# Performance work log

Hardware: AMD Instinct MI355X
Metric: run time of the kernel (lower is better)

The kernel has to match this reference:

```python
import jax, jax.numpy as jnp
import numpy as np

N_GRAPHS = 8
NODES_PER_G = 4096
N = N_GRAPHS * NODES_PER_G        # 32768 total nodes in the batched graph
E = N * 16                        # 524288 edges (avg degree 16)
F_IN = 128
HID = 64
FC_HID = 128
OUT = 2
SLOPE = 0.01                      # torch LeakyReLU default


def leaky_relu(x):
    return jnp.where(x >= 0, x, SLOPE * x)


def gcn_conv(x, W, b, src, dst, w, n_nodes):
    """PyG GCNConv with edge_weight: x' = D^-1/2 (A+I) D^-1/2 (x W) + b.
    Self-loops added with weight 1 (PyG default fill_value)."""
    xw = x @ W                                         # [N, out]
    deg = jax.ops.segment_sum(w, dst, num_segments=n_nodes) + 1.0  # +1 self-loop
    dinv = jnp.where(deg > 0, jax.lax.rsqrt(deg), 0.0)
    norm = dinv[src] * w * dinv[dst]                   # [E]
    agg = jax.ops.segment_sum(xw[src] * norm[:, None], dst, num_segments=n_nodes)
    agg = agg + xw * (dinv * dinv)[:, None]            # self-loop contribution
    return agg + b


def setup_inputs() -> dict:
    key = jax.random.key(0)
    ks = jax.random.split(key, 11)
    s = 0.05
    return {
        "x": jax.random.normal(ks[0], (N, F_IN), jnp.float32),
        "edge_index": jax.random.randint(ks[1], (2, E), 0, N, dtype=jnp.int32),
        "edge_attr": jax.random.uniform(ks[2], (E, 2), jnp.float32),
        "W1": jax.random.normal(ks[3], (F_IN, HID), jnp.float32) * s,
        "b1": jnp.zeros((HID,), jnp.float32),
        "W2": jax.random.normal(ks[4], (HID, 1), jnp.float32) * s,
        "b2": jnp.zeros((1,), jnp.float32),
        "fc1_W": jax.random.normal(ks[5], (NODES_PER_G, FC_HID), jnp.float32) * s,
        "fc1_b": jnp.zeros((FC_HID,), jnp.float32),
        "fc2_W": jax.random.normal(ks[6], (FC_HID, OUT), jnp.float32) * s,
        "fc2_b": jnp.zeros((OUT,), jnp.float32),
        "num_graphs": N_GRAPHS,
    }


def reference(x, edge_index, edge_attr, W1, b1, W2, b2, fc1_W, fc1_b, fc2_W, fc2_b, num_graphs):
    src, dst = edge_index[0], edge_index[1]
    w = edge_attr[:, 0]
    n = x.shape[0]
    h = leaky_relu(gcn_conv(x, W1, b1, src, dst, w, n))   # [N, 64]
    h = leaky_relu(gcn_conv(h, W2, b2, src, dst, w, n))   # [N, 1]
    out = h.reshape(num_graphs, -1)                       # [G, nodes_per_graph]
    out = leaky_relu(out @ fc1_W + fc1_b)                 # [G, 128]
    out = out @ fc2_W + fc2_b                             # [G, out_channels]
    return jax.nn.softmax(out, axis=1)
```

## Files before the change

kernel.cpp:

```cpp
#include <hip/hip_runtime.h>
#include <hip/hip_fp16.h>

#define F_IN 128
#define HID 64
#define FC_HID 128
#define NOUT 2
#define NGR 8
#define SLOPE 0.01f
#define SLOTS 64
#define NPB 256
#define NBUCK 256
#define DPB 128
#define SCAP 32
#define SEPT 8
#define ROWS_PB 16
#define XS_STR 132

__global__ __launch_bounds__(256) void fused_pg_kernel(const int* __restrict__ src,
                                                       const int* __restrict__ dst,
                                                       const float* __restrict__ edge_attr,
                                                       int* __restrict__ cntMat,
                                                       int2* __restrict__ staged, int E,
                                                       const float* __restrict__ x,
                                                       const float* __restrict__ W1,
                                                       __half* __restrict__ xwhr, int N,
                                                       int* __restrict__ zeroRegion,
                                                       int zeroInts) {
    __shared__ union {
        struct { float xs[64 * XS_STR]; float wl[F_IN * HID]; } g;
        struct { int cur[NBUCK]; } p;
    } sm;
    int tid = threadIdx.x;
    int bid = blockIdx.x;

    if (bid < NPB) {
        if (bid == 0) {
            for (int i = tid; i < zeroInts; i += 256) zeroRegion[i] = 0;
        }
        for (int i = tid; i < NBUCK; i += 256) sm.p.cur[i] = 0;
        __syncthreads();

        int base = (bid * 256 + tid) * SEPT;
        int s[SEPT], d[SEPT]; float w[SEPT]; int n = 0;
        if (base + SEPT <= E) {
            int4 sa = *(const int4*)(src + base);
            int4 sb = *(const int4*)(src + base + 4);
            int4 da = *(const int4*)(dst + base);
            int4 db = *(const int4*)(dst + base + 4);
            float4 a0 = *(const float4*)(edge_attr + (size_t)2 * base);
            float4 a1 = *(const float4*)(edge_attr + (size_t)2 * base + 4);
            float4 a2 = *(const float4*)(edge_attr + (size_t)2 * base + 8);
            float4 a3 = *(const float4*)(edge_attr + (size_t)2 * base + 12);
            s[0]=sa.x; s[1]=sa.y; s[2]=sa.z; s[3]=sa.w;
            s[4]=sb.x; s[5]=sb.y; s[6]=sb.z; s[7]=sb.w;
            d[0]=da.x; d[1]=da.y; d[2]=da.z; d[3]=da.w;
            d[4]=db.x; d[5]=db.y; d[6]=db.z; d[7]=db.w;
            w[0]=a0.x; w[1]=a0.z; w[2]=a1.x; w[3]=a1.z;
            w[4]=a2.x; w[5]=a2.z; w[6]=a3.x; w[7]=a3.z;
            n = SEPT;
        } else {
            for (int e = base; e < E && n < SEPT; ++e) {
                s[n] = src[e]; d[n] = dst[e]; w[n] = edge_attr[(size_t)2 * e]; ++n;
            }
        }

        #pragma unroll
        for (int k = 0; k < SEPT; ++k) {
            if (k < n) {
                int bk = d[k] >> 7;
                int pos = atomicAdd(&sm.p.cur[bk], 1);
                if (pos < SCAP)
                    staged[((size_t)bk * NPB + bid) * SCAP + pos] =
                        make_int2(((d[k] & (DPB - 1)) << 25) | s[k], __float_as_int(w[k]));
            }
        }
        __syncthreads();
        for (int i = tid; i < NBUCK; i += 256) {
            int c = sm.p.cur[i];
            cntMat[bid * NBUCK + i] = (c > SCAP) ? SCAP : c;
        }
        return;
    }

    int rowBase = (bid - NPB) * 64;
    if (rowBase >= N) return;

    #pragma unroll
    for (int i = 0; i < 8; ++i) {
        int f = tid + i * 256;
        *(float4*)&sm.g.wl[f * 4] = *(const float4*)&W1[f * 4];
    }
    #pragma unroll
    for (int i = 0; i < 8; ++i) {
        int f = tid + i * 256;
        int r = f >> 5, q = f & 31;
        if (rowBase + r < N)
            *(float4*)&sm.g.xs[r * XS_STR + q * 4] =
                *(const float4*)&x[(size_t)(rowBase + r) * F_IN + q * 4];
    }
    __syncthreads();

    int tr = tid & 15;
    int tc = tid >> 4;

    float4 acc0 = {0,0,0,0}, acc1 = {0,0,0,0}, acc2 = {0,0,0,0}, acc3 = {0,0,0,0};
    #pragma unroll 2
    for (int k = 0; k < F_IN; k += 4) {
        float4 a0 = *(const float4*)&sm.g.xs[(tr     ) * XS_STR + k];
        float4 a1 = *(const float4*)&sm.g.xs[(tr + 16) * XS_STR + k];
        float4 a2 = *(const float4*)&sm.g.xs[(tr + 32) * XS_STR + k];
        float4 a3 = *(const float4*)&sm.g.xs[(tr + 48) * XS_STR + k];
        float4 w0 = *(const float4*)&sm.g.wl[(k    ) * HID + tc * 4];
        float4 w1 = *(const float4*)&sm.g.wl[(k + 1) * HID + tc * 4];
        float4 w2 = *(const float4*)&sm.g.wl[(k + 2) * HID + tc * 4];
        float4 w3 = *(const float4*)&sm.g.wl[(k + 3) * HID + tc * 4];
        acc0.x += a0.x*w0.x + a0.y*w1.x + a0.z*w2.x + a0.w*w3.x;
        acc0.y += a0.x*w0.y + a0.y*w1.y + a0.z*w2.y + a0.w*w3.y;
        acc0.z += a0.x*w0.z + a0.y*w1.z + a0.z*w2.z + a0.w*w3.z;
        acc0.w += a0.x*w0.w + a0.y*w1.w + a0.z*w2.w + a0.w*w3.w;
        acc1.x += a1.x*w0.x + a1.y*w1.x + a1.z*w2.x + a1.w*w3.x;
        acc1.y += a1.x*w0.y + a1.y*w1.y + a1.z*w2.y + a1.w*w3.y;
        acc1.z += a1.x*w0.z + a1.y*w1.z + a1.z*w2.z + a1.w*w3.z;
        acc1.w += a1.x*w0.w + a1.y*w1.w + a1.z*w2.w + a1.w*w3.w;
        acc2.x += a2.x*w0.x + a2.y*w1.x + a2.z*w2.x + a2.w*w3.x;
        acc2.y += a2.x*w0.y + a2.y*w1.y + a2.z*w2.y + a2.w*w3.y;
        acc2.z += a2.x*w0.z + a2.y*w1.z + a2.z*w2.z + a2.w*w3.z;
        acc2.w += a2.x*w0.w + a2.y*w1.w + a2.z*w2.w + a2.w*w3.w;
        acc3.x += a3.x*w0.x + a3.y*w1.x + a3.z*w2.x + a3.w*w3.x;
        acc3.y += a3.x*w0.y + a3.y*w1.y + a3.z*w2.y + a3.w*w3.y;
        acc3.z += a3.x*w0.z + a3.y*w1.z + a3.z*w2.z + a3.w*w3.z;
        acc3.w += a3.x*w0.w + a3.y*w1.w + a3.z*w2.w + a3.w*w3.w;
    }

    int row0 = rowBase + tr;
    #define ST_H4(row, a)                                                            \
        if ((row) < N) {                                                             \
            __half2* p2 = (__half2*)&xwhr[(size_t)(row) * HID + tc * 4];             \
            p2[0] = __floats2half2_rn(a.x, a.y);                                     \
            p2[1] = __floats2half2_rn(a.z, a.w);                                     \
        }
    ST_H4(row0,      acc0)
    ST_H4(row0 + 16, acc1)
    ST_H4(row0 + 32, acc2)
    ST_H4(row0 + 48, acc3)
    #undef ST_H4
}

__global__ __launch_bounds__(256) void build_kernel(const int2* __restrict__ staged,
                                                    const int* __restrict__ cntMat,
                                                    int2* __restrict__ slots,
                                                    int* __restrict__ cnt,
                                                    float* __restrict__ dinv,
                                                    const __half* __restrict__ xwhr,
                                                    __half* __restrict__ xwh) {
    __shared__ int2 lsl[DPB * SLOTS];
    __shared__ int lcur[DPB];
    __shared__ float lsum[DPB];
    int b = blockIdx.x;
    int tid = threadIdx.x;
    if (tid < DPB) { lcur[tid] = 0; lsum[tid] = 0.0f; }
    __syncthreads();

    int c_kb = cntMat[tid * NBUCK + b];
    const int2* sp = staged + ((size_t)b * NPB + tid) * SCAP;
    for (int i = 0; i < c_kb; ++i) {
        int2 rec = sp[i];
        int d = (rec.x >> 25) & (DPB - 1);
        atomicAdd(&lsum[d], __int_as_float(rec.y));
        int pos = atomicAdd(&lcur[d], 1);
        if (pos < SLOTS) lsl[d * SLOTS + pos] = make_int2(rec.x & 0x1FFFFFF, rec.y);
    }
    __syncthreads();

    const int4* lv = (const int4*)lsl;
    int4* gv = (int4*)(slots + (size_t)b * DPB * SLOTS);
    #pragma unroll 4
    for (int i = tid; i < DPB * SLOTS / 2; i += 256) gv[i] = lv[i];

    if (tid < DPB) {
        int c = lcur[tid];
        cnt[b * DPB + tid] = (c > SLOTS) ? SLOTS : c;
        float di = rsqrtf(lsum[tid] + 1.0f);
        dinv[b * DPB + tid] = di;
        lsum[tid] = di;
    }
    __syncthreads();

    const __half2* xr2 = (const __half2*)(xwhr + (size_t)b * DPB * HID);
    __half2* xh2 = (__half2*)(xwh + (size_t)b * DPB * HID);
    for (int i = tid; i < DPB * HID / 2; i += 256) {
        float di = lsum[i >> 5];
        float2 v = __half22float2(xr2[i]);
        xh2[i] = __floats2half2_rn(v.x * di, v.y * di);
    }
}

__global__ __launch_bounds__(256) void gather1_kernel(const int2* __restrict__ slots,
                                                      const int* __restrict__ cnt,
                                                      const float* __restrict__ dinv,
                                                      const __half* __restrict__ xwh,
                                                      const float* __restrict__ b1,
                                                      const float* __restrict__ W2,
                                                      float* __restrict__ hwS, int N) {
    int d = blockIdx.x * 4 + (threadIdx.x >> 6);
    if (d >= N) return;
    int lane = threadIdx.x & 63;
    int c = cnt[d];

    int sidx = 0, wbits = 0;
    if (lane < c) {
        int2 sw = slots[(size_t)d * SLOTS + lane];
        sidx  = sw.x;
        wbits = sw.y;
    }
    float di   = dinv[d];
    float self = __half2float(xwh[(size_t)d * HID + lane]);

    float acc0 = 0.0f, acc1 = 0.0f, acc2 = 0.0f, acc3 = 0.0f;
    int i = 0;
    for (; i + 7 < c; i += 8) {
        int s0 = __builtin_amdgcn_readlane(sidx, i + 0);
        int s1 = __builtin_amdgcn_readlane(sidx, i + 1);
        int s2 = __builtin_amdgcn_readlane(sidx, i + 2);
        int s3 = __builtin_amdgcn_readlane(sidx, i + 3);
        int s4 = __builtin_amdgcn_readlane(sidx, i + 4);
        int s5 = __builtin_amdgcn_readlane(sidx, i + 5);
        int s6 = __builtin_amdgcn_readlane(sidx, i + 6);
        int s7 = __builtin_amdgcn_readlane(sidx, i + 7);
        float n0 = __int_as_float(__builtin_amdgcn_readlane(wbits, i + 0));
        float n1 = __int_as_float(__builtin_amdgcn_readlane(wbits, i + 1));
        float n2 = __int_as_float(__builtin_amdgcn_readlane(wbits, i + 2));
        float n3 = __int_as_float(__builtin_amdgcn_readlane(wbits, i + 3));
        float n4 = __int_as_float(__builtin_amdgcn_readlane(wbits, i + 4));
        float n5 = __int_as_float(__builtin_amdgcn_readlane(wbits, i + 5));
        float n6 = __int_as_float(__builtin_amdgcn_readlane(wbits, i + 6));
        float n7 = __int_as_float(__builtin_amdgcn_readlane(wbits, i + 7));
        float v0 = __half2float(xwh[(size_t)s0 * HID + lane]);
        float v1 = __half2float(xwh[(size_t)s1 * HID + lane]);
        float v2 = __half2float(xwh[(size_t)s2 * HID + lane]);
        float v3 = __half2float(xwh[(size_t)s3 * HID + lane]);
        float v4 = __half2float(xwh[(size_t)s4 * HID + lane]);
        float v5 = __half2float(xwh[(size_t)s5 * HID + lane]);
        float v6 = __half2float(xwh[(size_t)s6 * HID + lane]);
        float v7 = __half2float(xwh[(size_t)s7 * HID + lane]);
        acc0 += v0 * n0; acc1 += v1 * n1; acc2 += v2 * n2; acc3 += v3 * n3;
        acc0 += v4 * n4; acc1 += v5 * n5; acc2 += v6 * n6; acc3 += v7 * n7;
    }
    for (; i < c; ++i) {
        int sI   = __builtin_amdgcn_readlane(sidx, i);
        float nI = __int_as_float(__builtin_amdgcn_readlane(wbits, i));
        acc0 += __half2float(xwh[(size_t)sI * HID + lane]) * nI;
    }
    float acc = (acc0 + acc1) + (acc2 + acc3);

    float v = acc * di + self * di + b1[lane];
    v = (v >= 0.0f) ? v : SLOPE * v;
    float p = v * W2[lane];
    #pragma unroll
    for (int m = 32; m >= 1; m >>= 1)
        p += __shfl_xor(p, m, 64);
    if (lane == 0) hwS[d] = p * di;
}

__global__ __launch_bounds__(256) void g2fc_kernel(const int2* __restrict__ slots,
                                                   const int* __restrict__ cnt,
                                                   const float* __restrict__ dinv,
                                                   const float* __restrict__ hwS,
                                                   const float* __restrict__ b2,
                                                   const float* __restrict__ fc1_W,
                                                   float* __restrict__ fc1out,
                                                   int* __restrict__ ticket,
                                                   const float* __restrict__ fc1_b,
                                                   const float* __restrict__ fc2_W,
                                                   const float* __restrict__ fc2_b,
                                                   float* __restrict__ out,
                                                   int nodesPerG) {
    __shared__ float hs[NGR][ROWS_PB];
    __shared__ float p1s[NGR][FC_HID];
    __shared__ float hid[NGR][FC_HID];
    __shared__ float outs[NGR * NOUT];
    __shared__ int lastFlag;

    int tid  = threadIdx.x;
    int row0 = blockIdx.x * ROWS_PB;

    if (tid < NGR * ROWS_PB) {
        int g = tid >> 4, r = tid & 15;
        int d = g * nodesPerG + row0 + r;
        int c = cnt[d];
        float di   = dinv[d];
        float self = hwS[d];
        const int4* sp4 = (const int4*)(slots + (size_t)d * SLOTS);
        float acc0 = 0.0f, acc1 = 0.0f;
        int i = 0;
        for (; i + 8 <= c; i += 8) {
            int4 q0 = sp4[(i >> 1) + 0];
            int4 q1 = sp4[(i >> 1) + 1];
            int4 q2 = sp4[(i >> 1) + 2];
            int4 q3 = sp4[(i >> 1) + 3];
            float v0 = hwS[q0.x], v1 = hwS[q0.z];
            float v2 = hwS[q1.x], v3 = hwS[q1.z];
            float v4 = hwS[q2.x], v5 = hwS[q2.z];
            float v6 = hwS[q3.x], v7 = hwS[q3.z];
            acc0 += v0 * __int_as_float(q0.y) + v1 * __int_as_float(q0.w);
            acc1 += v2 * __int_as_float(q1.y) + v3 * __int_as_float(q1.w);
            acc0 += v4 * __int_as_float(q2.y) + v5 * __int_as_float(q2.w);
            acc1 += v6 * __int_as_float(q3.y) + v7 * __int_as_float(q3.w);
        }
        const int2* sp = (const int2*)sp4;
        for (; i < c; ++i) {
            int2 sw = sp[i];
            acc0 += hwS[sw.x] * __int_as_float(sw.y);
        }
        float v = (acc0 + acc1) * di + self * di + b2[0];
        hs[g][r] = (v >= 0.0f) ? v : SLOPE * v;
    }
    __syncthreads();

    int j = tid & 127, half = tid >> 7;
    float acc[NGR];
    #pragma unroll
    for (int g = 0; g < NGR; ++g) acc[g] = 0.0f;
    for (int r = half * 8; r < half * 8 + 8; ++r) {
        float wv = fc1_W[(size_t)(row0 + r) * FC_HID + j];
        #pragma unroll
        for (int g = 0; g < NGR; ++g) acc[g] += hs[g][r] * wv;
    }
    if (half == 1) {
        #pragma unroll
        for (int g = 0; g < NGR; ++g) p1s[g][j] = acc[g];
    }
    __syncthreads();
    if (half == 0) {
        #pragma unroll
        for (int g = 0; g < NGR; ++g)
            atomicAdd(&fc1out[g * FC_HID + j], acc[g] + p1s[g][j]);
    }

    __threadfence();
    if (tid == 0) lastFlag = (atomicAdd(ticket, 1) == (int)gridDim.x - 1);
    __syncthreads();
    if (!lastFlag) return;
    __threadfence();

    if (tid < FC_HID) {
        #pragma unroll
        for (int g = 0; g < NGR; ++g) {
            float v = atomicAdd(&fc1out[g * FC_HID + tid], 0.0f) + fc1_b[tid];
            hid[g][tid] = (v >= 0.0f) ? v : SLOPE * v;
        }
    }
    __syncthreads();
    if (tid < NGR * NOUT) {
        int g = tid >> 1, o = tid & 1;
        float a = fc2_b[o];
        #pragma unroll
        for (int k = 0; k < FC_HID; ++k)
            a += hid[g][k] * fc2_W[(size_t)k * NOUT + o];
        outs[tid] = a;
    }
    __syncthreads();
    if (tid < NGR) {
        float o0 = outs[tid * 2], o1 = outs[tid * 2 + 1];
        float m = fmaxf(o0, o1);
        float e0 = __expf(o0 - m), e1 = __expf(o1 - m);
        float s = e0 + e1;
        out[(size_t)tid * NOUT + 0] = e0 / s;
        out[(size_t)tid * NOUT + 1] = e1 / s;
    }
}

extern "C" void kernel_launch(void* const* d_in, const int* in_sizes, int n_in,
                              void* d_out, int out_size, void* d_ws, size_t ws_size,
                              hipStream_t stream) {
    const float* x          = (const float*)d_in[0];
    const int*   edge_index = (const int*)d_in[1];
    const float* edge_attr  = (const float*)d_in[2];
    const float* W1         = (const float*)d_in[3];
    const float* b1         = (const float*)d_in[4];
    const float* W2         = (const float*)d_in[5];
    const float* b2         = (const float*)d_in[6];
    const float* fc1_W      = (const float*)d_in[7];
    const float* fc1_b      = (const float*)d_in[8];
    const float* fc2_W      = (const float*)d_in[9];
    const float* fc2_b      = (const float*)d_in[10];
    float* out = (float*)d_out;

    int N = in_sizes[0] / F_IN;
    int E = in_sizes[1] / 2;
    int nodesPerG = in_sizes[7] / FC_HID;

    const int* src = edge_index;
    const int* dst = edge_index + E;

    char* wsb = (char*)d_ws;
    float* fc1out = (float*)wsb;
    int*   ticket = (int*)(wsb + (size_t)NGR * FC_HID * 4);
    int zeroInts  = NGR * FC_HID + 1;
    size_t off = ((size_t)NGR * FC_HID * 4 + 16 + 255) & ~255ull;
    int*   cntMat = (int*)(wsb + off);
    int2*  staged = (int2*)(wsb + off + (size_t)NPB * NBUCK * 4);
    int2*  slots  = staged + (size_t)NBUCK * NPB * SCAP;
    __half* xwhr  = (__half*)(slots + (size_t)N * SLOTS);
    __half* xwh   = xwhr + (size_t)N * HID;
    float* dinv   = (float*)(xwh + (size_t)N * HID);
    float* hwS    = dinv + N;
    int*   cnt    = (int*)(hwS + N);

    int gemmB = (N + 63) / 64;
    fused_pg_kernel<<<NPB + gemmB, 256, 0, stream>>>(src, dst, edge_attr, cntMat, staged, E,
                                                     x, W1, xwhr, N, (int*)fc1out, zeroInts);
    build_kernel<<<NBUCK, 256, 0, stream>>>(staged, cntMat, slots, cnt, dinv, xwhr, xwh);
    gather1_kernel<<<(N + 3) / 4, 256, 0, stream>>>(slots, cnt, dinv, xwh, b1, W2, hwS, N);
    g2fc_kernel<<<nodesPerG / ROWS_PB, 256, 0, stream>>>(slots, cnt, dinv, hwS, b2,
                                                         fc1_W, fc1out, ticket,
                                                         fc1_b, fc2_W, fc2_b, out, nodesPerG);
}
```

Measured before the change: 81.34 us.

## Process two nodes per wave in layer-1 gather with half2 feature loads

Restructures the layer-1 gather so each 64-lane wave handles two destination nodes, with 32 lanes per node each loading a half2 (two features) instead of one half per lane. Neighbor indices and weights are broadcast within each half-wave via shuffles, and edges beyond 32 per node fall back to direct slot reads. This aims to widen memory accesses and halve the number of waves, cutting per-node wave overhead for low-degree nodes. In exchange it adds divergence when the two nodes differ in degree, uses shuffles instead of scalar readlanes, and unrolls by 4 instead of 8.

After: 84.16 us. 1.03x slower.

```diff
diff --git a/kernel.cpp b/kernel.cpp
--- a/kernel.cpp
+++ b/kernel.cpp
@@ -202,64 +202,77 @@
                                                       const float* __restrict__ b1,
                                                       const float* __restrict__ W2,
                                                       float* __restrict__ hwS, int N) {
-    int d = blockIdx.x * 4 + (threadIdx.x >> 6);
-    if (d >= N) return;
+    int wave = (blockIdx.x * 256 + threadIdx.x) >> 6;
     int lane = threadIdx.x & 63;
-    int c = cnt[d];
-
+    int fl   = lane & 31;
+    int node = wave * 2 + (lane >> 5);
+    if (node >= N) return;
+
+    int c_my = cnt[node];
     int sidx = 0, wbits = 0;
-    if (lane < c) {
-        int2 sw = slots[(size_t)d * SLOTS + lane];
-        sidx  = sw.x;
-        wbits = sw.y;
-    }
-    float di   = dinv[d];
-    float self = __half2float(xwh[(size_t)d * HID + lane]);
-
-    float acc0 = 0.0f, acc1 = 0.0f, acc2 = 0.0f, acc3 = 0.0f;
+    if (fl < c_my) {
+        int2 sw = slots[(size_t)node * SLOTS + fl];
+        sidx = sw.x; wbits = sw.y;
+    }
+    float di = dinv[node];
+    float2 self = __half22float2(*(const __half2*)&xwh[(size_t)node * HID + fl * 2]);
+
+    int cA = __shfl(c_my, 0, 64);
+    int cB = __shfl(c_my, 32, 64);
+    int cmax = (cA > cB) ? cA : cB; if (cmax > 32) cmax = 32;
+    int hbase = lane & 32;
+
+    float2 acc0 = {0,0}, acc1 = {0,0}, acc2 = {0,0}, acc3 = {0,0};
     int i = 0;
-    for (; i + 7 < c; i += 8) {
-        int s0 = __builtin_amdgcn_readlane(sidx, i + 0);
-        int s1 = __builtin_amdgcn_readlane(sidx, i + 1);
-        int s2 = __builtin_amdgcn_readlane(sidx, i + 2);
-        int s3 = __builtin_amdgcn_readlane(sidx, i + 3);
-        int s4 = __builtin_amdgcn_readlane(sidx, i + 4);
-        int s5 = __builtin_amdgcn_readlane(sidx, i + 5);
-        int s6 = __builtin_amdgcn_readlane(sidx, i + 6);
-        int s7 = __builtin_amdgcn_readlane(sidx, i + 7);
-        float n0 = __int_as_float(__builtin_amdgcn_readlane(wbits, i + 0));
-        float n1 = __int_as_float(__builtin_amdgcn_readlane(wbits, i + 1));
-        float n2 = __int_as_float(__builtin_amdgcn_readlane(wbits, i + 2));
-        float n3 = __int_as_float(__builtin_amdgcn_readlane(wbits, i + 3));
-        float n4 = __int_as_float(__builtin_amdgcn_readlane(wbits, i + 4));
-        float n5 = __int_as_float(__builtin_amdgcn_readlane(wbits, i + 5));
-        float n6 = __int_as_float(__builtin_amdgcn_readlane(wbits, i + 6));
-        float n7 = __int_as_float(__builtin_amdgcn_readlane(wbits, i + 7));
-        float v0 = __half2float(xwh[(size_t)s0 * HID + lane]);
-        float v1 = __half2float(xwh[(size_t)s1 * HID + lane]);
-        float v2 = __half2float(xwh[(size_t)s2 * HID + lane]);
-        float v3 = __half2float(xwh[(size_t)s3 * HID + lane]);
-        float v4 = __half2float(xwh[(size_t)s4 * HID + lane]);
-        float v5 = __half2float(xwh[(size_t)s5 * HID + lane]);
-        float v6 = __half2float(xwh[(size_t)s6 * HID + lane]);
-        float v7 = __half2float(xwh[(size_t)s7 * HID + lane]);
-        acc0 += v0 * n0; acc1 += v1 * n1; acc2 += v2 * n2; acc3 += v3 * n3;
-        acc0 += v4 * n4; acc1 += v5 * n5; acc2 += v6 * n6; acc3 += v7 * n7;
-    }
-    for (; i < c; ++i) {
-        int sI   = __builtin_amdgcn_readlane(sidx, i);
-        float nI = __int_as_float(__builtin_amdgcn_readlane(wbits, i));
-        acc0 += __half2float(xwh[(size_t)sI * HID + lane]) * nI;
-    }
-    float acc = (acc0 + acc1) + (acc2 + acc3);
-
-    float v = acc * di + self * di + b1[lane];
-    v = (v >= 0.0f) ? v : SLOPE * v;
-    float p = v * W2[lane];
+    for (; i + 3 < cmax; i += 4) {
+        int s0 = __shfl(sidx, hbase + i,     64); int w0 = __shfl(wbits, hbase + i,     64);
+        int s1 = __shfl(sidx, hbase + i + 1, 64); int w1 = __shfl(wbits, hbase + i + 1, 64);
+        int s2 = __shfl(sidx, hbase + i + 2, 64); int w2 = __shfl(wbits, hbase + i + 2, 64);
+        int s3 = __shfl(sidx, hbase + i + 3, 64); int w3 = __shfl(wbits, hbase + i + 3, 64);
+        if (i + 0 < c_my) {
+            float2 v = __half22float2(*(const __half2*)&xwh[(size_t)s0 * HID + fl * 2]);
+            float n = __int_as_float(w0); acc0.x += v.x * n; acc0.y += v.y * n;
+        }
+        if (i + 1 < c_my) {
+            float2 v = __half22float2(*(const __half2*)&xwh[(size_t)s1 * HID + fl * 2]);
+            float n = __int_as_float(w1); acc1.x += v.x * n; acc1.y += v.y * n;
+        }
+        if (i + 2 < c_my) {
+            float2 v = __half22float2(*(const __half2*)&xwh[(size_t)s2 * HID + fl * 2]);
+            float n = __int_as_float(w2); acc2.x += v.x * n; acc2.y += v.y * n;
+        }
+        if (i + 3 < c_my) {
+            float2 v = __half22float2(*(const __half2*)&xwh[(size_t)s3 * HID + fl * 2]);
+            float n = __int_as_float(w3); acc3.x += v.x * n; acc3.y += v.y * n;
+        }
+    }
+    for (; i < cmax; ++i) {
+        int sI = __shfl(sidx, hbase + i, 64); int wI = __shfl(wbits, hbase + i, 64);
+        if (i < c_my) {
+            float2 v = __half22float2(*(const __half2*)&xwh[(size_t)sI * HID + fl * 2]);
+            float n = __int_as_float(wI); acc0.x += v.x * n; acc0.y += v.y * n;
+        }
+    }
+    for (int j = 32; j < c_my; ++j) {
+        int2 sw = slots[(size_t)node * SLOTS + j];
+        float n = __int_as_float(sw.y);
+        float2 v = __half22float2(*(const __half2*)&xwh[(size_t)sw.x * HID + fl * 2]);
+        acc0.x += v.x * n; acc0.y += v.y * n;
+    }
+
+    float ax = (acc0.x + acc1.x) + (acc2.x + acc3.x);
+    float ay = (acc0.y + acc1.y) + (acc2.y + acc3.y);
+    float2 b1v = *(const float2*)&b1[fl * 2];
+    float vx = ax * di + self.x * di + b1v.x;
+    float vy = ay * di + self.y * di + b1v.y;
+    vx = (vx >= 0.0f) ? vx : SLOPE * vx;
+    vy = (vy >= 0.0f) ? vy : SLOPE * vy;
+    float2 w2v = *(const float2*)&W2[fl * 2];
+    float p = vx * w2v.x + vy * w2v.y;
     #pragma unroll
-    for (int m = 32; m >= 1; m >>= 1)
+    for (int m = 16; m >= 1; m >>= 1)
         p += __shfl_xor(p, m, 64);
-    if (lane == 0) hwS[d] = p * di;
+    if (fl == 0) hwS[node] = p * di;
 }
 
 __global__ __launch_bounds__(256) void g2fc_kernel(const int2* __restrict__ slots,
@@ -411,7 +424,7 @@
     fused_pg_kernel<<<NPB + gemmB, 256, 0, stream>>>(src, dst, edge_attr, cntMat, staged, E,
                                                      x, W1, xwhr, N, (int*)fc1out, zeroInts);
     build_kernel<<<NBUCK, 256, 0, stream>>>(staged, cntMat, slots, cnt, dinv, xwhr, xwh);
-    gather1_kernel<<<(N + 3) / 4, 256, 0, stream>>>(slots, cnt, dinv, xwh, b1, W2, hwS, N);
+    gather1_kernel<<<(N / 2 + 3) / 4, 256, 0, stream>>>(slots, cnt, dinv, xwh, b1, W2, hwS, N);
     g2fc_kernel<<<nodesPerG / ROWS_PB, 256, 0, stream>>>(slots, cnt, dinv, hwS, b2,
                                                          fc1_W, fc1out, ticket,
                                                          fc1_b, fc2_W, fc2_b, out, nodesPerG);
```
